# Kernel tuning notes

Hardware: AMD Instinct MI355X
Metric: run time of the kernel (lower is better)

Reference implementation:

```python
import jax, jax.numpy as jnp
import numpy as np

S = 64.0   # scale (default s)
M = 0.5    # angular margin (default m)
EPS = 1e-07
N, D, C = 2048, 128, 100000

def setup_inputs() -> dict:
    key = jax.random.key(0)
    kx, kw, kl = jax.random.split(key, 3)
    x = jax.random.normal(kx, (N, D), dtype=jnp.float32)
    # NOTE: the torch module never actually normalizes W (local rebinding bug),
    # so W is a raw linear weight. Small init keeps exp(s*wf) finite.
    W = jax.random.normal(kw, (C, D), dtype=jnp.float32) * 0.01
    labels = jax.random.randint(kl, (N,), 0, C, dtype=jnp.int64)
    return {"x": x, "W": W, "labels": labels}

def reference(x, W, labels):
    # L2-normalize embeddings only (matches original: weight normalize is a no-op)
    x_n = x / jnp.linalg.norm(x, axis=1, keepdims=True)
    wf = jnp.einsum('nd,cd->nc', x_n, W)                      # [N, C] logits
    tgt = jnp.take_along_axis(wf, labels[:, None], axis=1)[:, 0]  # wf[i, y_i]
    tgt = jnp.clip(tgt, -1.0 + EPS, 1.0 - EPS)
    numerator = S * jnp.cos(jnp.arccos(tgt) + M)              # margin logit
    # sum over j != y_i of exp(s * wf_ij)
    exp_all = jnp.exp(S * wf)
    excl_sum = jnp.sum(exp_all, axis=1) - jnp.take_along_axis(exp_all, labels[:, None], axis=1)[:, 0]
    denominator = jnp.exp(numerator) + excl_sum
    L = numerator - jnp.log(denominator)
    return -jnp.mean(L)
```

## Files before the change

### kernel.cpp

```cpp
#include <hip/hip_runtime.h>
#include <math.h>

typedef __attribute__((ext_vector_type(8))) short s16x8;
typedef __attribute__((ext_vector_type(4))) float f32x4;

#define N_ROWS 2048
#define D_DIM  128
#define N_CLS  100000
#define N_TILES 782
#define N_PAD   96.0f
#define S_SCALE 64.0f
#define S_LOG2E 92.33248261689366f
#define EPS_F   1e-7f
#define COS_M   0.8775825618903728f
#define SIN_M   0.479425538604203f

#if __has_builtin(__builtin_amdgcn_exp2f)
#define EXP2F(x) __builtin_amdgcn_exp2f(x)
#else
#define EXP2F(x) exp2f(x)
#endif

__device__ __forceinline__ unsigned int f2bf1(float f) {
    unsigned int u = __float_as_uint(f);
    return (u + 0x7FFFu + ((u >> 16) & 1u)) >> 16;
}
__device__ __forceinline__ unsigned int f2bf2(float lo, float hi) {
    return f2bf1(lo) | (f2bf1(hi) << 16);
}

__global__ __launch_bounds__(256)
void k_normalize(const float* __restrict__ x, const float* __restrict__ W,
                 const int* __restrict__ labels,
                 float* __restrict__ tgt, uint4* __restrict__ xb2) {
    const int gt = blockIdx.x;
    const int t = threadIdx.x;
    const int rr = t >> 1, h = t & 1;
    const int row = gt * 128 + rr;

    const f32x4* src = (const f32x4*)(x + (size_t)row * D_DIM + h * 64);
    f32x4 v[16];
    float s = 0.f;
    #pragma unroll
    for (int q = 0; q < 16; q++) {
        v[q] = src[q];
        s += v[q][0]*v[q][0] + v[q][1]*v[q][1] + v[q][2]*v[q][2] + v[q][3]*v[q][3];
    }
    s += __shfl_xor(s, 1);
    const float inv = 1.0f / sqrtf(s);

    const int y = labels[row];
    const f32x4* wsrc = (const f32x4*)(W + (size_t)y * D_DIM + h * 64);
    float d = 0.f;
    #pragma unroll
    for (int q = 0; q < 16; q++) {
        f32x4 w = wsrc[q];
        d += v[q][0]*w[0] + v[q][1]*w[1] + v[q][2]*w[2] + v[q][3]*w[3];
    }
    d += __shfl_xor(d, 1);
    if (h == 0) tgt[row] = d * inv;

    #pragma unroll
    for (int q = 0; q < 16; q++) {
        v[q][0] *= inv; v[q][1] *= inv; v[q][2] *= inv; v[q][3] *= inv;
    }

    const int wn = rr >> 6, j = (rr >> 4) & 3, lr = rr & 15;
    #pragma unroll
    for (int q2 = 0; q2 < 8; q2++) {
        const int ck = h * 8 + q2;
        const int ks = ck >> 2, lk = ck & 3;
        const int idx = gt * 2048 + wn * 1024 + j * 256 + ks * 64 + lk * 16 + lr;
        f32x4 f0 = v[q2 * 2], f1 = v[q2 * 2 + 1];
        xb2[idx] = make_uint4(f2bf2(f0[0], f0[1]), f2bf2(f0[2], f0[3]),
                              f2bf2(f1[0], f1[1]), f2bf2(f1[2], f1[3]));
    }
}

#define PHASE(BCUR, BNEXT, IT, J, ITN, JN, LAST) do {                        \
    if (!(LAST)) {                                                            \
        _Pragma("unroll")                                                     \
        for (int ks_ = 0; ks_ < 4; ks_++)                                     \
            BNEXT[ks_] = bbase[(ITN) * 2048 + (JN) * 256 + ks_ * 64];         \
    }                                                                         \
    f32x4 acc0 = {0.f,0.f,0.f,0.f}, acc1 = {0.f,0.f,0.f,0.f};                 \
    f32x4 acc2 = {0.f,0.f,0.f,0.f}, acc3 = {0.f,0.f,0.f,0.f};                 \
    _Pragma("unroll")                                                         \
    for (int ks_ = 0; ks_ < 4; ks_++) {                                       \
        const s16x8 b_ = *(const s16x8*)&BCUR[ks_];                           \
        acc0 = __builtin_amdgcn_mfma_f32_16x16x32_bf16(a_[ks_][0], b_, acc0, 0, 0, 0); \
        acc1 = __builtin_amdgcn_mfma_f32_16x16x32_bf16(a_[ks_][1], b_, acc1, 0, 0, 0); \
        acc2 = __builtin_amdgcn_mfma_f32_16x16x32_bf16(a_[ks_][2], b_, acc2, 0, 0, 0); \
        acc3 = __builtin_amdgcn_mfma_f32_16x16x32_bf16(a_[ks_][3], b_, acc3, 0, 0, 0); \
    }                                                                         \
    float pj = 0.f;                                                           \
    _Pragma("unroll")                                                         \
    for (int r_ = 0; r_ < 4; r_++)                                            \
        pj += EXP2F(S_LOG2E * acc0[r_]) + EXP2F(S_LOG2E * acc1[r_])           \
            + EXP2F(S_LOG2E * acc2[r_]) + EXP2F(S_LOG2E * acc3[r_]);          \
    pj += __shfl_xor(pj, 16);                                                 \
    pj += __shfl_xor(pj, 32);                                                 \
    if ((lane >> 4) == 0)                                                     \
        psum[wm][IT][wn * 64 + (J) * 16 + lr] = pj;                           \
} while (0)

__global__ __launch_bounds__(256, 3)
void k_main(const uint4* __restrict__ xb2, const float* __restrict__ W,
            float* __restrict__ rowsum) {
    __shared__ uint4 Wsh[2048];
    __shared__ float psum[2][16][128];
    const int t = threadIdx.x;
    const int c0 = blockIdx.x * 128;

    #pragma unroll
    for (int m = 0; m < 8; m++) {
        const int idx = m * 256 + t;
        const int flr = idx & 15, lk = (idx >> 4) & 3;
        const int ks = (idx >> 6) & 3, fi = (idx >> 8) & 3, fwm = idx >> 10;
        const int cls = c0 + fwm * 64 + fi * 16 + flr;
        const int k0 = (ks * 4 + lk) * 8;
        uint4 val = make_uint4(0u, 0u, 0u, 0u);
        if (cls < N_CLS) {
            const f32x4* g = (const f32x4*)(W + (size_t)cls * D_DIM + k0);
            f32x4 f0 = g[0], f1 = g[1];
            val.x = f2bf2(f0[0], f0[1]); val.y = f2bf2(f0[2], f0[3]);
            val.z = f2bf2(f1[0], f1[1]); val.w = f2bf2(f1[2], f1[3]);
        }
        Wsh[idx] = val;
    }
    __syncthreads();

    const int lane = t & 63;
    const int wid = t >> 6;
    const int wm = wid >> 1;
    const int wn = wid & 1;
    const int lr = lane & 15;
    const uint4* bbase = xb2 + wn * 1024 + lane;

    uint4 bA[4], bB[4];
    s16x8 a_[4][4];

    #pragma unroll
    for (int ks = 0; ks < 4; ks++) bA[ks] = bbase[ks * 64];

    for (int it = 0; it < 16; it++) {
        #pragma unroll
        for (int ks = 0; ks < 4; ks++)
            #pragma unroll
            for (int i = 0; i < 4; i++)
                a_[ks][i] = *(const s16x8*)&Wsh[wm * 1024 + i * 256 + ks * 64 + lane];
        PHASE(bA, bB, it, 0, it, 1, false);
        PHASE(bB, bA, it, 1, it, 2, false);
        PHASE(bA, bB, it, 2, it, 3, false);
        PHASE(bB, bA, it, 3, it + 1, 0, it == 15);
    }

    __syncthreads();
    #pragma unroll
    for (int k = 0; k < 8; k++) {
        const int flat = t + k * 256;
        const int it = flat >> 7, r = flat & 127;
        atomicAdd(&rowsum[it * 128 + r], psum[0][it][r] + psum[1][it][r]);
    }
}

__global__ void k_final(const float* __restrict__ rowsum, const float* __restrict__ tgt,
                        float* __restrict__ out) {
    int t = threadIdx.x;
    float lsum = 0.f;
    for (int i = t; i < N_ROWS; i += 256) {
        float tr = tgt[i];
        float tc = fminf(fmaxf(tr, -1.f + EPS_F), 1.f - EPS_F);
        float num = S_SCALE * (tc * COS_M - sqrtf(fmaxf(1.f - tc * tc, 0.f)) * SIN_M);
        float excl = rowsum[i] - N_PAD - __expf(S_SCALE * tr);
        float den = __expf(num) + excl;
        lsum += num - logf(den);
    }
    #pragma unroll
    for (int off = 1; off < 64; off <<= 1) lsum += __shfl_xor(lsum, off);
    __shared__ float wsums[4];
    if ((t & 63) == 0) wsums[t >> 6] = lsum;
    __syncthreads();
    if (t == 0) out[0] = -(wsums[0] + wsums[1] + wsums[2] + wsums[3]) / (float)N_ROWS;
}

extern "C" void kernel_launch(void* const* d_in, const int* in_sizes, int n_in,
                              void* d_out, int out_size, void* d_ws, size_t ws_size,
                              hipStream_t stream) {
    const float* x = (const float*)d_in[0];
    const float* W = (const float*)d_in[1];
    const int* labels = (const int*)d_in[2];
    float* out = (float*)d_out;

    uint4* xb2    = (uint4*)d_ws;
    float* rowsum = (float*)((char*)xb2 + (size_t)N_ROWS * D_DIM * 2);
    float* tgt    = rowsum + N_ROWS;

    hipMemsetAsync(rowsum, 0, N_ROWS * sizeof(float), stream);
    k_normalize<<<N_ROWS / 128, 256, 0, stream>>>(x, W, labels, tgt, xb2);
    k_main<<<N_TILES, 256, 0, stream>>>(xb2, W, rowsum);
    k_final<<<1, 256, 0, stream>>>(rowsum, tgt, out);
}
```

Measured before the change: 93.13 us.

## Keep W fragments in registers, fold scale into x, deepen B prefetch

Each wave now loads its bf16 W fragments straight from global memory into registers once, instead of staging them in a shared-memory tile and re-reading them every iteration. The S*log2e factor is folded into the normalized x during preprocessing, which removes a multiply per exp in the hot loop. The B operand is now prefetched four phases ahead in four register buffers, and partial row sums go through LDS atomics into a single psum array. Register pressure rises, so the occupancy hint drops from 3 to 2 blocks per CU. Scaling x before the bf16 conversion also slightly changes rounding.

```diff
diff --git a/kernel.cpp b/kernel.cpp
--- a/kernel.cpp
+++ b/kernel.cpp
@@ -60,9 +60,10 @@
     d += __shfl_xor(d, 1);
     if (h == 0) tgt[row] = d * inv;
 
+    const float invs = inv * S_LOG2E;
     #pragma unroll
     for (int q = 0; q < 16; q++) {
-        v[q][0] *= inv; v[q][1] *= inv; v[q][2] *= inv; v[q][3] *= inv;
+        v[q][0] *= invs; v[q][1] *= invs; v[q][2] *= invs; v[q][3] *= invs;
     }
 
     const int wn = rr >> 6, j = (rr >> 4) & 3, lr = rr & 15;
@@ -77,82 +78,85 @@
     }
 }
 
-#define PHASE(BCUR, BNEXT, IT, J, ITN, JN, LAST) do {                        \
-    if (!(LAST)) {                                                            \
-        _Pragma("unroll")                                                     \
-        for (int ks_ = 0; ks_ < 4; ks_++)                                     \
-            BNEXT[ks_] = bbase[(ITN) * 2048 + (JN) * 256 + ks_ * 64];         \
-    }                                                                         \
+#define PH(BUF, J) do {                                                       \
     f32x4 acc0 = {0.f,0.f,0.f,0.f}, acc1 = {0.f,0.f,0.f,0.f};                 \
     f32x4 acc2 = {0.f,0.f,0.f,0.f}, acc3 = {0.f,0.f,0.f,0.f};                 \
     _Pragma("unroll")                                                         \
     for (int ks_ = 0; ks_ < 4; ks_++) {                                       \
-        const s16x8 b_ = *(const s16x8*)&BCUR[ks_];                           \
+        const s16x8 b_ = *(const s16x8*)&BUF[ks_];                            \
         acc0 = __builtin_amdgcn_mfma_f32_16x16x32_bf16(a_[ks_][0], b_, acc0, 0, 0, 0); \
         acc1 = __builtin_amdgcn_mfma_f32_16x16x32_bf16(a_[ks_][1], b_, acc1, 0, 0, 0); \
         acc2 = __builtin_amdgcn_mfma_f32_16x16x32_bf16(a_[ks_][2], b_, acc2, 0, 0, 0); \
         acc3 = __builtin_amdgcn_mfma_f32_16x16x32_bf16(a_[ks_][3], b_, acc3, 0, 0, 0); \
     }                                                                         \
-    float pj = 0.f;                                                           \
+    if (it < 15) {                                                            \
+        _Pragma("unroll")                                                     \
+        for (int ks_ = 0; ks_ < 4; ks_++)                                     \
+            BUF[ks_] = bbase[(it + 1) * 2048 + (J) * 256 + ks_ * 64];         \
+    }                                                                         \
+    f32x4 pv;                                                                 \
     _Pragma("unroll")                                                         \
     for (int r_ = 0; r_ < 4; r_++)                                            \
-        pj += EXP2F(S_LOG2E * acc0[r_]) + EXP2F(S_LOG2E * acc1[r_])           \
-            + EXP2F(S_LOG2E * acc2[r_]) + EXP2F(S_LOG2E * acc3[r_]);          \
+        pv[r_] = (EXP2F(acc0[r_]) + EXP2F(acc1[r_]))                          \
+               + (EXP2F(acc2[r_]) + EXP2F(acc3[r_]));                         \
+    float pj = (pv[0] + pv[1]) + (pv[2] + pv[3]);                             \
     pj += __shfl_xor(pj, 16);                                                 \
     pj += __shfl_xor(pj, 32);                                                 \
     if ((lane >> 4) == 0)                                                     \
-        psum[wm][IT][wn * 64 + (J) * 16 + lr] = pj;                           \
+        atomicAdd(&psum[it][wn * 64 + (J) * 16 + lr], pj);                    \
 } while (0)
 
-__global__ __launch_bounds__(256, 3)
+__global__ __launch_bounds__(256, 2)
 void k_main(const uint4* __restrict__ xb2, const float* __restrict__ W,
             float* __restrict__ rowsum) {
-    __shared__ uint4 Wsh[2048];
-    __shared__ float psum[2][16][128];
+    __shared__ float psum[16][128];
     const int t = threadIdx.x;
     const int c0 = blockIdx.x * 128;
-
-    #pragma unroll
-    for (int m = 0; m < 8; m++) {
-        const int idx = m * 256 + t;
-        const int flr = idx & 15, lk = (idx >> 4) & 3;
-        const int ks = (idx >> 6) & 3, fi = (idx >> 8) & 3, fwm = idx >> 10;
-        const int cls = c0 + fwm * 64 + fi * 16 + flr;
-        const int k0 = (ks * 4 + lk) * 8;
-        uint4 val = make_uint4(0u, 0u, 0u, 0u);
-        if (cls < N_CLS) {
-            const f32x4* g = (const f32x4*)(W + (size_t)cls * D_DIM + k0);
-            f32x4 f0 = g[0], f1 = g[1];
-            val.x = f2bf2(f0[0], f0[1]); val.y = f2bf2(f0[2], f0[3]);
-            val.z = f2bf2(f1[0], f1[1]); val.w = f2bf2(f1[2], f1[3]);
-        }
-        Wsh[idx] = val;
-    }
-    __syncthreads();
 
     const int lane = t & 63;
     const int wid = t >> 6;
     const int wm = wid >> 1;
     const int wn = wid & 1;
     const int lr = lane & 15;
+    const int lk = lane >> 4;
+
+    #pragma unroll
+    for (int k = 0; k < 8; k++) ((float*)psum)[t + k * 256] = 0.f;
+
+    s16x8 a_[4][4];
+    #pragma unroll
+    for (int ks = 0; ks < 4; ks++)
+        #pragma unroll
+        for (int i = 0; i < 4; i++) {
+            const int cls = c0 + wm * 64 + i * 16 + lr;
+            uint4 val = make_uint4(0u, 0u, 0u, 0u);
+            if (cls < N_CLS) {
+                const f32x4* g = (const f32x4*)(W + (size_t)cls * D_DIM + (ks * 4 + lk) * 8);
+                f32x4 f0 = g[0], f1 = g[1];
+                val.x = f2bf2(f0[0], f0[1]); val.y = f2bf2(f0[2], f0[3]);
+                val.z = f2bf2(f1[0], f1[1]); val.w = f2bf2(f1[2], f1[3]);
+            }
+            a_[ks][i] = *(s16x8*)&val;
+        }
+
     const uint4* bbase = xb2 + wn * 1024 + lane;
 
-    uint4 bA[4], bB[4];
-    s16x8 a_[4][4];
-
-    #pragma unroll
-    for (int ks = 0; ks < 4; ks++) bA[ks] = bbase[ks * 64];
+    uint4 b0[4], b1[4], b2[4], b3[4];
+    #pragma unroll
+    for (int ks = 0; ks < 4; ks++) {
+        b0[ks] = bbase[0 * 256 + ks * 64];
+        b1[ks] = bbase[1 * 256 + ks * 64];
+        b2[ks] = bbase[2 * 256 + ks * 64];
+        b3[ks] = bbase[3 * 256 + ks * 64];
+    }
+
+    __syncthreads();
 
     for (int it = 0; it < 16; it++) {
-        #pragma unroll
-        for (int ks = 0; ks < 4; ks++)
-            #pragma unroll
-            for (int i = 0; i < 4; i++)
-                a_[ks][i] = *(const s16x8*)&Wsh[wm * 1024 + i * 256 + ks * 64 + lane];
-        PHASE(bA, bB, it, 0, it, 1, false);
-        PHASE(bB, bA, it, 1, it, 2, false);
-        PHASE(bA, bB, it, 2, it, 3, false);
-        PHASE(bB, bA, it, 3, it + 1, 0, it == 15);
+        PH(b0, 0);
+        PH(b1, 1);
+        PH(b2, 2);
+        PH(b3, 3);
     }
 
     __syncthreads();
@@ -160,7 +164,7 @@
     for (int k = 0; k < 8; k++) {
         const int flat = t + k * 256;
         const int it = flat >> 7, r = flat & 127;
-        atomicAdd(&rowsum[it * 128 + r], psum[0][it][r] + psum[1][it][r]);
+        atomicAdd(&rowsum[it * 128 + r], psum[it][r]);
     }
 }
 
```

Measured after the change: 100.1 us. +7.5%, slower.

## Software-pipeline MFMA and exp epilogue with ping-pong accumulators, fold scale into x

Applied to the files above, without the earlier changes.

Moves the S*log2e scale into the normalized x before bf16 conversion, so the exp2 in the epilogue needs no extra multiply. Restructures the main loop with two accumulator sets so the exp/reduce of one 16-column block overlaps the MFMAs of the next. It also keeps four B buffers in registers and prefetches a full iteration ahead. This raises register pressure under the 3-blocks-per-SM launch bound and may cause spills. Folding the scale before bf16 rounding slightly changes numerics.

```diff
diff --git a/kernel.cpp b/kernel.cpp
--- a/kernel.cpp
+++ b/kernel.cpp
@@ -60,9 +60,10 @@
     d += __shfl_xor(d, 1);
     if (h == 0) tgt[row] = d * inv;
 
+    const float invs = inv * S_LOG2E;
     #pragma unroll
     for (int q = 0; q < 16; q++) {
-        v[q][0] *= inv; v[q][1] *= inv; v[q][2] *= inv; v[q][3] *= inv;
+        v[q][0] *= invs; v[q][1] *= invs; v[q][2] *= invs; v[q][3] *= invs;
     }
 
     const int wn = rr >> 6, j = (rr >> 4) & 3, lr = rr & 15;
@@ -77,31 +78,38 @@
     }
 }
 
-#define PHASE(BCUR, BNEXT, IT, J, ITN, JN, LAST) do {                        \
-    if (!(LAST)) {                                                            \
+#define MFMA16(ACC, BUF) do {                                                 \
+    ACC##0 = (f32x4){0.f,0.f,0.f,0.f}; ACC##1 = (f32x4){0.f,0.f,0.f,0.f};     \
+    ACC##2 = (f32x4){0.f,0.f,0.f,0.f}; ACC##3 = (f32x4){0.f,0.f,0.f,0.f};     \
+    _Pragma("unroll")                                                         \
+    for (int ks_ = 0; ks_ < 4; ks_++) {                                       \
+        const s16x8 b_ = *(const s16x8*)&BUF[ks_];                            \
+        ACC##0 = __builtin_amdgcn_mfma_f32_16x16x32_bf16(a_[ks_][0], b_, ACC##0, 0, 0, 0); \
+        ACC##1 = __builtin_amdgcn_mfma_f32_16x16x32_bf16(a_[ks_][1], b_, ACC##1, 0, 0, 0); \
+        ACC##2 = __builtin_amdgcn_mfma_f32_16x16x32_bf16(a_[ks_][2], b_, ACC##2, 0, 0, 0); \
+        ACC##3 = __builtin_amdgcn_mfma_f32_16x16x32_bf16(a_[ks_][3], b_, ACC##3, 0, 0, 0); \
+    }                                                                         \
+} while (0)
+
+#define RELOAD(BUF, J) do {                                                   \
+    if (it < 15) {                                                            \
         _Pragma("unroll")                                                     \
         for (int ks_ = 0; ks_ < 4; ks_++)                                     \
-            BNEXT[ks_] = bbase[(ITN) * 2048 + (JN) * 256 + ks_ * 64];         \
+            BUF[ks_] = bbase[(it + 1) * 2048 + (J) * 256 + ks_ * 64];         \
     }                                                                         \
-    f32x4 acc0 = {0.f,0.f,0.f,0.f}, acc1 = {0.f,0.f,0.f,0.f};                 \
-    f32x4 acc2 = {0.f,0.f,0.f,0.f}, acc3 = {0.f,0.f,0.f,0.f};                 \
-    _Pragma("unroll")                                                         \
-    for (int ks_ = 0; ks_ < 4; ks_++) {                                       \
-        const s16x8 b_ = *(const s16x8*)&BCUR[ks_];                           \
-        acc0 = __builtin_amdgcn_mfma_f32_16x16x32_bf16(a_[ks_][0], b_, acc0, 0, 0, 0); \
-        acc1 = __builtin_amdgcn_mfma_f32_16x16x32_bf16(a_[ks_][1], b_, acc1, 0, 0, 0); \
-        acc2 = __builtin_amdgcn_mfma_f32_16x16x32_bf16(a_[ks_][2], b_, acc2, 0, 0, 0); \
-        acc3 = __builtin_amdgcn_mfma_f32_16x16x32_bf16(a_[ks_][3], b_, acc3, 0, 0, 0); \
-    }                                                                         \
-    float pj = 0.f;                                                           \
+} while (0)
+
+#define EXPST(ACC, ITE, JE) do {                                              \
+    f32x4 pv;                                                                 \
     _Pragma("unroll")                                                         \
     for (int r_ = 0; r_ < 4; r_++)                                            \
-        pj += EXP2F(S_LOG2E * acc0[r_]) + EXP2F(S_LOG2E * acc1[r_])           \
-            + EXP2F(S_LOG2E * acc2[r_]) + EXP2F(S_LOG2E * acc3[r_]);          \
+        pv[r_] = (EXP2F(ACC##0[r_]) + EXP2F(ACC##1[r_]))                      \
+               + (EXP2F(ACC##2[r_]) + EXP2F(ACC##3[r_]));                     \
+    float pj = (pv[0] + pv[1]) + (pv[2] + pv[3]);                             \
     pj += __shfl_xor(pj, 16);                                                 \
     pj += __shfl_xor(pj, 32);                                                 \
     if ((lane >> 4) == 0)                                                     \
-        psum[wm][IT][wn * 64 + (J) * 16 + lr] = pj;                           \
+        psum[wm][ITE][wn * 64 + (JE) * 16 + lr] = pj;                         \
 } while (0)
 
 __global__ __launch_bounds__(256, 3)
@@ -137,11 +145,18 @@
     const int lr = lane & 15;
     const uint4* bbase = xb2 + wn * 1024 + lane;
 
-    uint4 bA[4], bB[4];
+    uint4 b0[4], b1[4], b2[4], b3[4];
     s16x8 a_[4][4];
-
-    #pragma unroll
-    for (int ks = 0; ks < 4; ks++) bA[ks] = bbase[ks * 64];
+    f32x4 accA0, accA1, accA2, accA3;
+    f32x4 accB0, accB1, accB2, accB3;
+
+    #pragma unroll
+    for (int ks = 0; ks < 4; ks++) {
+        b0[ks] = bbase[0 * 256 + ks * 64];
+        b1[ks] = bbase[1 * 256 + ks * 64];
+        b2[ks] = bbase[2 * 256 + ks * 64];
+        b3[ks] = bbase[3 * 256 + ks * 64];
+    }
 
     for (int it = 0; it < 16; it++) {
         #pragma unroll
@@ -149,11 +164,13 @@
             #pragma unroll
             for (int i = 0; i < 4; i++)
                 a_[ks][i] = *(const s16x8*)&Wsh[wm * 1024 + i * 256 + ks * 64 + lane];
-        PHASE(bA, bB, it, 0, it, 1, false);
-        PHASE(bB, bA, it, 1, it, 2, false);
-        PHASE(bA, bB, it, 2, it, 3, false);
-        PHASE(bB, bA, it, 3, it + 1, 0, it == 15);
-    }
+        if (it) EXPST(accB, it - 1, 3);
+        MFMA16(accA, b0);  RELOAD(b0, 0);
+        MFMA16(accB, b1);  RELOAD(b1, 1);  EXPST(accA, it, 0);
+        MFMA16(accA, b2);  RELOAD(b2, 2);  EXPST(accB, it, 1);
+        MFMA16(accB, b3);  RELOAD(b3, 3);  EXPST(accA, it, 2);
+    }
+    EXPST(accB, 15, 3);
 
     __syncthreads();
     #pragma unroll
```

Result: slower. 96.23 us (+3.3%).

## Switch main GEMM to 32x32x16 MFMA with new layout and prescaled embeddings

Applied to the files above, without the earlier changes.

The main kernel moves from 16x16x32 MFMA tiles to 32x32x16 tiles. Each wave now covers 32 rows against all 128 classes of the block and reads the A operands straight from shared memory on each k-step instead of keeping them in registers. The normalize kernel folds the s*log2(e) scale into the bf16 embeddings, which removes a multiply before each exp2, and it is relaid out with 8 threads per row and more blocks. The intent is fewer MFMA instructions, less register pressure and a simpler psum reduction, at the cost of more LDS reads per iteration and bf16 rounding of the scaled values.

```diff
diff --git a/kernel.cpp b/kernel.cpp
--- a/kernel.cpp
+++ b/kernel.cpp
@@ -3,6 +3,7 @@
 
 typedef __attribute__((ext_vector_type(8))) short s16x8;
 typedef __attribute__((ext_vector_type(4))) float f32x4;
+typedef __attribute__((ext_vector_type(16))) float f32x16;
 
 #define N_ROWS 2048
 #define D_DIM  128
@@ -21,6 +22,8 @@
 #define EXP2F(x) exp2f(x)
 #endif
 
+#define ZERO16 {0.f,0.f,0.f,0.f,0.f,0.f,0.f,0.f,0.f,0.f,0.f,0.f,0.f,0.f,0.f,0.f}
+
 __device__ __forceinline__ unsigned int f2bf1(float f) {
     unsigned int u = __float_as_uint(f);
     return (u + 0x7FFFu + ((u >> 16) & 1u)) >> 16;
@@ -33,92 +36,89 @@
 void k_normalize(const float* __restrict__ x, const float* __restrict__ W,
                  const int* __restrict__ labels,
                  float* __restrict__ tgt, uint4* __restrict__ xb2) {
-    const int gt = blockIdx.x;
     const int t = threadIdx.x;
-    const int rr = t >> 1, h = t & 1;
-    const int row = gt * 128 + rr;
+    const int row = blockIdx.x * 32 + (t >> 3);
+    const int p = t & 7;
 
-    const f32x4* src = (const f32x4*)(x + (size_t)row * D_DIM + h * 64);
-    f32x4 v[16];
+    const f32x4* src = (const f32x4*)(x + (size_t)row * D_DIM + p * 16);
+    f32x4 v[4];
     float s = 0.f;
     #pragma unroll
-    for (int q = 0; q < 16; q++) {
+    for (int q = 0; q < 4; q++) {
         v[q] = src[q];
         s += v[q][0]*v[q][0] + v[q][1]*v[q][1] + v[q][2]*v[q][2] + v[q][3]*v[q][3];
     }
-    s += __shfl_xor(s, 1);
+    s += __shfl_xor(s, 1); s += __shfl_xor(s, 2); s += __shfl_xor(s, 4);
     const float inv = 1.0f / sqrtf(s);
 
     const int y = labels[row];
-    const f32x4* wsrc = (const f32x4*)(W + (size_t)y * D_DIM + h * 64);
+    const f32x4* wsrc = (const f32x4*)(W + (size_t)y * D_DIM + p * 16);
     float d = 0.f;
     #pragma unroll
-    for (int q = 0; q < 16; q++) {
+    for (int q = 0; q < 4; q++) {
         f32x4 w = wsrc[q];
         d += v[q][0]*w[0] + v[q][1]*w[1] + v[q][2]*w[2] + v[q][3]*w[3];
     }
-    d += __shfl_xor(d, 1);
-    if (h == 0) tgt[row] = d * inv;
+    d += __shfl_xor(d, 1); d += __shfl_xor(d, 2); d += __shfl_xor(d, 4);
+    if (p == 0) tgt[row] = d * inv;
 
+    const float invs = inv * S_LOG2E;
     #pragma unroll
-    for (int q = 0; q < 16; q++) {
-        v[q][0] *= inv; v[q][1] *= inv; v[q][2] *= inv; v[q][3] *= inv;
+    for (int q = 0; q < 4; q++) {
+        v[q][0] *= invs; v[q][1] *= invs; v[q][2] *= invs; v[q][3] *= invs;
     }
 
-    const int wn = rr >> 6, j = (rr >> 4) & 3, lr = rr & 15;
+    const int it = row >> 7, wq = (row >> 5) & 3, r32 = row & 31;
     #pragma unroll
-    for (int q2 = 0; q2 < 8; q2++) {
-        const int ck = h * 8 + q2;
-        const int ks = ck >> 2, lk = ck & 3;
-        const int idx = gt * 2048 + wn * 1024 + j * 256 + ks * 64 + lk * 16 + lr;
-        f32x4 f0 = v[q2 * 2], f1 = v[q2 * 2 + 1];
+    for (int kh = 0; kh < 2; kh++) {
+        const int idx = it * 2048 + wq * 512 + p * 64 + kh * 32 + r32;
+        f32x4 f0 = v[kh * 2], f1 = v[kh * 2 + 1];
         xb2[idx] = make_uint4(f2bf2(f0[0], f0[1]), f2bf2(f0[2], f0[3]),
                               f2bf2(f1[0], f1[1]), f2bf2(f1[2], f1[3]));
     }
 }
 
-#define PHASE(BCUR, BNEXT, IT, J, ITN, JN, LAST) do {                        \
-    if (!(LAST)) {                                                            \
-        _Pragma("unroll")                                                     \
-        for (int ks_ = 0; ks_ < 4; ks_++)                                     \
-            BNEXT[ks_] = bbase[(ITN) * 2048 + (JN) * 256 + ks_ * 64];         \
+#define ITBODY(BCUR, BNXT, IT) do {                                           \
+    f32x16 acc0 = ZERO16, acc1 = ZERO16, acc2 = ZERO16, acc3 = ZERO16;        \
+    _Pragma("unroll")                                                         \
+    for (int kt = 0; kt < 8; kt++) {                                          \
+        const s16x8 a0 = *(const s16x8*)&Wsh[0 * 512 + kt * 64 + lane];       \
+        const s16x8 a1 = *(const s16x8*)&Wsh[1 * 512 + kt * 64 + lane];       \
+        const s16x8 a2 = *(const s16x8*)&Wsh[2 * 512 + kt * 64 + lane];       \
+        const s16x8 a3 = *(const s16x8*)&Wsh[3 * 512 + kt * 64 + lane];       \
+        const s16x8 b_ = *(const s16x8*)&BCUR[kt];                            \
+        acc0 = __builtin_amdgcn_mfma_f32_32x32x16_bf16(a0, b_, acc0, 0, 0, 0);\
+        acc1 = __builtin_amdgcn_mfma_f32_32x32x16_bf16(a1, b_, acc1, 0, 0, 0);\
+        acc2 = __builtin_amdgcn_mfma_f32_32x32x16_bf16(a2, b_, acc2, 0, 0, 0);\
+        acc3 = __builtin_amdgcn_mfma_f32_32x32x16_bf16(a3, b_, acc3, 0, 0, 0);\
+        if ((IT) + 1 < 16)                                                    \
+            BNXT[kt] = bbase[((IT) + 1) * 2048 + kt * 64];                    \
     }                                                                         \
-    f32x4 acc0 = {0.f,0.f,0.f,0.f}, acc1 = {0.f,0.f,0.f,0.f};                 \
-    f32x4 acc2 = {0.f,0.f,0.f,0.f}, acc3 = {0.f,0.f,0.f,0.f};                 \
+    float sA = 0.f, sB = 0.f;                                                 \
     _Pragma("unroll")                                                         \
-    for (int ks_ = 0; ks_ < 4; ks_++) {                                       \
-        const s16x8 b_ = *(const s16x8*)&BCUR[ks_];                           \
-        acc0 = __builtin_amdgcn_mfma_f32_16x16x32_bf16(a_[ks_][0], b_, acc0, 0, 0, 0); \
-        acc1 = __builtin_amdgcn_mfma_f32_16x16x32_bf16(a_[ks_][1], b_, acc1, 0, 0, 0); \
-        acc2 = __builtin_amdgcn_mfma_f32_16x16x32_bf16(a_[ks_][2], b_, acc2, 0, 0, 0); \
-        acc3 = __builtin_amdgcn_mfma_f32_16x16x32_bf16(a_[ks_][3], b_, acc3, 0, 0, 0); \
+    for (int r_ = 0; r_ < 16; r_++) {                                         \
+        sA += EXP2F(acc0[r_]) + EXP2F(acc1[r_]);                              \
+        sB += EXP2F(acc2[r_]) + EXP2F(acc3[r_]);                              \
     }                                                                         \
-    float pj = 0.f;                                                           \
-    _Pragma("unroll")                                                         \
-    for (int r_ = 0; r_ < 4; r_++)                                            \
-        pj += EXP2F(S_LOG2E * acc0[r_]) + EXP2F(S_LOG2E * acc1[r_])           \
-            + EXP2F(S_LOG2E * acc2[r_]) + EXP2F(S_LOG2E * acc3[r_]);          \
-    pj += __shfl_xor(pj, 16);                                                 \
-    pj += __shfl_xor(pj, 32);                                                 \
-    if ((lane >> 4) == 0)                                                     \
-        psum[wm][IT][wn * 64 + (J) * 16 + lr] = pj;                           \
+    float s_ = sA + sB;                                                       \
+    s_ += __shfl_xor(s_, 32);                                                 \
+    if (lane < 32) psum[IT][wq * 32 + lane] = s_;                             \
 } while (0)
 
 __global__ __launch_bounds__(256, 3)
 void k_main(const uint4* __restrict__ xb2, const float* __restrict__ W,
             float* __restrict__ rowsum) {
     __shared__ uint4 Wsh[2048];
-    __shared__ float psum[2][16][128];
+    __shared__ float psum[16][128];
     const int t = threadIdx.x;
     const int c0 = blockIdx.x * 128;
 
     #pragma unroll
     for (int m = 0; m < 8; m++) {
         const int idx = m * 256 + t;
-        const int flr = idx & 15, lk = (idx >> 4) & 3;
-        const int ks = (idx >> 6) & 3, fi = (idx >> 8) & 3, fwm = idx >> 10;
-        const int cls = c0 + fwm * 64 + fi * 16 + flr;
-        const int k0 = (ks * 4 + lk) * 8;
+        const int ct = idx >> 9, kt = (idx >> 6) & 7, ln = idx & 63;
+        const int cls = c0 + ct * 32 + (ln & 31);
+        const int k0 = kt * 16 + (ln >> 5) * 8;
         uint4 val = make_uint4(0u, 0u, 0u, 0u);
         if (cls < N_CLS) {
             const f32x4* g = (const f32x4*)(W + (size_t)cls * D_DIM + k0);
@@ -131,36 +131,24 @@
     __syncthreads();
 
     const int lane = t & 63;
-    const int wid = t >> 6;
-    const int wm = wid >> 1;
-    const int wn = wid & 1;
-    const int lr = lane & 15;
-    const uint4* bbase = xb2 + wn * 1024 + lane;
+    const int wq = t >> 6;
+    const uint4* bbase = xb2 + wq * 512 + lane;
 
-    uint4 bA[4], bB[4];
-    s16x8 a_[4][4];
+    uint4 bP[8], bQ[8];
+    #pragma unroll
+    for (int kt = 0; kt < 8; kt++) bP[kt] = bbase[kt * 64];
 
-    #pragma unroll
-    for (int ks = 0; ks < 4; ks++) bA[ks] = bbase[ks * 64];
-
-    for (int it = 0; it < 16; it++) {
-        #pragma unroll
-        for (int ks = 0; ks < 4; ks++)
-            #pragma unroll
-            for (int i = 0; i < 4; i++)
-                a_[ks][i] = *(const s16x8*)&Wsh[wm * 1024 + i * 256 + ks * 64 + lane];
-        PHASE(bA, bB, it, 0, it, 1, false);
-        PHASE(bB, bA, it, 1, it, 2, false);
-        PHASE(bA, bB, it, 2, it, 3, false);
-        PHASE(bB, bA, it, 3, it + 1, 0, it == 15);
+    for (int it = 0; it < 16; it += 2) {
+        ITBODY(bP, bQ, it);
+        ITBODY(bQ, bP, it + 1);
     }
 
     __syncthreads();
     #pragma unroll
     for (int k = 0; k < 8; k++) {
         const int flat = t + k * 256;
-        const int it = flat >> 7, r = flat & 127;
-        atomicAdd(&rowsum[it * 128 + r], psum[0][it][r] + psum[1][it][r]);
+        const int itg = flat >> 7, r = flat & 127;
+        atomicAdd(&rowsum[itg * 128 + r], psum[itg][r]);
     }
 }
 
@@ -197,7 +185,7 @@
     float* tgt    = rowsum + N_ROWS;
 
     hipMemsetAsync(rowsum, 0, N_ROWS * sizeof(float), stream);
-    k_normalize<<<N_ROWS / 128, 256, 0, stream>>>(x, W, labels, tgt, xb2);
+    k_normalize<<<N_ROWS / 32, 256, 0, stream>>>(x, W, labels, tgt, xb2);
     k_main<<<N_TILES, 256, 0, stream>>>(xb2, W, rowsum);
     k_final<<<1, 256, 0, stream>>>(rowsum, tgt, out);
 }
```

After: 274.5 us. +194.8%, slower.
